# Optimization experiments

Measured on AMD Instinct MI355X. Metric: run time of the kernel, lower is better.

Reference implementation:

```python
import jax, jax.numpy as jnp
import numpy as np

NUM_RBF = 16
RBF_D_MIN, RBF_D_MAX = 2.0, 22.0
CB_A, CB_B, CB_C = -0.58273431, 0.56802827, -0.54067466
TOP_K = 32
MAX_REL = 32
NPOS = 16
HID = 128
LN_EPS = 1e-5


def _gather_nodes(nodes, idx):
    # nodes: (B, L, D), idx: (B, L, K) -> (B, L, K, D)
    return jax.vmap(lambda n, i: n[i])(nodes, idx)


def _rbf_encode(D):
    mu = jnp.linspace(RBF_D_MIN, RBF_D_MAX, NUM_RBF, dtype=D.dtype)
    sigma = (RBF_D_MAX - RBF_D_MIN) / NUM_RBF
    return jnp.exp(-((D[..., None] - mu) ** 2) / (sigma ** 2))


def setup_inputs() -> dict:
    key = jax.random.key(0)
    ks = jax.random.split(key, 4)
    B, L = 2, 2048
    X = jax.random.normal(ks[0], (B, L, 4, 3), jnp.float32) * 10.0
    residue_mask = jnp.ones((B, L), jnp.float32)
    R_idx = jnp.arange(B * L, dtype=jnp.int32).reshape(B, L)
    chain_labels = jnp.zeros((B, L), jnp.int32)
    # learned params
    W_pos = jax.random.normal(ks[1], (NPOS, 2 * MAX_REL + 2), jnp.float32) * 0.05
    b_pos = jnp.zeros((NPOS,), jnp.float32)
    W_edge = jax.random.normal(ks[2], (HID, 25 * NUM_RBF + NPOS), jnp.float32) * 0.02
    ln_gamma = jnp.ones((HID,), jnp.float32)
    ln_beta = jnp.zeros((HID,), jnp.float32)
    return {"X": X, "residue_mask": residue_mask, "R_idx": R_idx,
            "chain_labels": chain_labels, "W_pos": W_pos, "b_pos": b_pos,
            "W_edge": W_edge, "ln_gamma": ln_gamma, "ln_beta": ln_beta}


def reference(X, residue_mask, R_idx, chain_labels, W_pos, b_pos, W_edge, ln_gamma, ln_beta):
    B, L = X.shape[0], X.shape[1]
    K = min(TOP_K, L)
    # virtual CB from backbone N, CA, C
    N, CA, C = X[..., 0, :], X[..., 1, :], X[..., 2, :]
    b = CA - N
    c = C - CA
    a = jnp.cross(b, c, axis=-1)
    CB = (CB_A * a + CB_B * b + CB_C * c + CA)[..., None, :]
    atoms_5 = jnp.concatenate([X, CB], axis=-2)  # (B, L, 5, 3)
    # kNN on CA coords with invalid residues pushed far away
    diff = CA[:, :, None, :] - CA[:, None, :, :]
    dist_sq = jnp.sum(diff * diff, axis=-1)  # (B, L, L)
    inv_mask = 1.0 - residue_mask
    dist_sq = dist_sq + inv_mask[:, None, :] * 1e6
    _, E_idx = jax.lax.top_k(-dist_sq, K)  # smallest-k indices, (B, L, K)
    # gather neighbor 5-atom coords and compute 25 pairwise distances
    Xf = atoms_5.reshape(B, L, 15)
    Xg = _gather_nodes(Xf, E_idx).reshape(B, L, K, 5, 3)
    d2 = jnp.sum((atoms_5[:, :, None, :, None, :] - Xg[:, :, :, None, :, :]) ** 2, axis=-1)
    D = jnp.sqrt(d2 + 1e-6)  # (B, L, K, 5, 5)
    rbf = _rbf_encode(D).reshape(B, L, K, 25 * NUM_RBF)
    # positional encodings (standard ProteinMPNN form)
    Rg = _gather_nodes(R_idx[..., None], E_idx)[..., 0]  # (B, L, K)
    Cg = _gather_nodes(chain_labels[..., None], E_idx)[..., 0]
    d_rel = Rg - R_idx[:, :, None]
    same_chain = (Cg == chain_labels[:, :, None])
    d_clip = jnp.clip(d_rel + MAX_REL, 0, 2 * MAX_REL)
    d_final = jnp.where(same_chain, d_clip, 2 * MAX_REL + 1)
    oh = jax.nn.one_hot(d_final, 2 * MAX_REL + 2, dtype=rbf.dtype)
    pos_enc = jnp.einsum('blkc,pc->blkp', oh, W_pos) + b_pos
    # edge embedding + layernorm
    edge_input = jnp.concatenate([pos_enc, rbf], axis=-1)  # (B, L, K, 416)
    h = jnp.einsum('blkf,hf->blkh', edge_input, W_edge)
    mean = jnp.mean(h, axis=-1, keepdims=True)
    var = jnp.var(h, axis=-1, keepdims=True)
    E = (h - mean) * jax.lax.rsqrt(var + LN_EPS) * ln_gamma + ln_beta
    return E_idx, E
```

## Files before the change

### kernel.cpp

```cpp
#include <hip/hip_runtime.h>
#include <hip/hip_bf16.h>

#define LEN   2048
#define KNB   32
#define HID   128

typedef unsigned long long ull;
typedef unsigned int uint32;
typedef float f32x4 __attribute__((ext_vector_type(4)));

__global__ __launch_bounds__(256) void prep_kernel(
    const float* __restrict__ X, const float* __restrict__ mask,
    const float* __restrict__ W_edge,
    float4* __restrict__ CAm, int* __restrict__ Wf8) {
    const int t = blockIdx.x * 256 + threadIdx.x;
    if (t < 2 * LEN) {
        const float* p = X + (size_t)t * 12;
        CAm[t] = make_float4(p[3], p[4], p[5],
                             __fmul_rn(__fsub_rn(1.0f, mask[t]), 1000000.0f));
    }
    if (t < 13312) {
        const float4 w = ((const float4*)W_edge)[t];
        int r = __builtin_amdgcn_cvt_pk_fp8_f32(w.x, w.y, 0, false);
        r = __builtin_amdgcn_cvt_pk_fp8_f32(w.z, w.w, r, true);
        Wf8[t] = r;
    }
}

__global__ __launch_bounds__(256) void topk_kernel(
    const float4* __restrict__ CAm, float* __restrict__ eidx_out) {
    const int row = blockIdx.x;
    const int b = row >> 11;
    const int i = row & (LEN - 1);
    const int tid = threadIdx.x;

    __shared__ int hist[512];
    __shared__ ull cand[LEN];
    __shared__ int candcnt;
    __shared__ int selB;

    const float4* C = CAm + (size_t)b * LEN;
    const float4 ci = C[i];

    uint32 d2b[8];
#pragma unroll
    for (int q = 0; q < 8; ++q) {
        const float4 cj = C[q * 256 + tid];
        float dx = __fsub_rn(ci.x, cj.x);
        float dy = __fsub_rn(ci.y, cj.y);
        float dz = __fsub_rn(ci.z, cj.z);
        float d2 = __fadd_rn(__fadd_rn(__fmul_rn(dx, dx), __fmul_rn(dy, dy)),
                             __fmul_rn(dz, dz));
        d2 = __fadd_rn(d2, cj.w);
        d2b[q] = __float_as_uint(d2);
    }

    hist[tid] = 0; hist[tid + 256] = 0;
    if (tid == 0) candcnt = 0;
    __syncthreads();
#pragma unroll
    for (int q = 0; q < 8; ++q) atomicAdd(&hist[d2b[q] >> 22], 1);
    __syncthreads();

    if (tid < 64) {
        int loc[8];
        int s = 0;
#pragma unroll
        for (int t = 0; t < 8; ++t) { loc[t] = hist[tid * 8 + t]; s += loc[t]; }
        int incl = s;
#pragma unroll
        for (int off = 1; off < 64; off <<= 1) {
            int o = __shfl_up(incl, off, 64);
            if (tid >= off) incl += o;
        }
        const int excl = incl - s;
        if (excl < KNB && incl >= KNB) {
            int c = excl;
#pragma unroll
            for (int t = 0; t < 8; ++t) {
                int c2 = c + loc[t];
                if (c < KNB && c2 >= KNB) selB = tid * 8 + t;
                c = c2;
            }
        }
    }
    __syncthreads();
    const uint32 B = (uint32)selB;

#pragma unroll
    for (int q = 0; q < 8; ++q) {
        if ((d2b[q] >> 22) <= B) {
            int p = atomicAdd(&candcnt, 1);
            cand[p] = (((ull)d2b[q]) << 32) | (uint32)(q * 256 + tid);
        }
    }
    __syncthreads();
    const int M = candcnt;

    for (int c = tid; c < M; c += 256) {
        const ull k = cand[c];
        int r = 0;
        for (int m = 0; m < M; ++m) r += (cand[m] < k);
        if (r < KNB)
            eidx_out[(size_t)row * KNB + r] = (float)(uint32)(k & 0xFFFFFFFFull);
    }
}

__device__ __forceinline__ void load_res_atoms(const float* __restrict__ p, float* dst) {
    const float Nx = p[0], Ny = p[1], Nz = p[2];
    const float Ax = p[3], Ay = p[4], Az = p[5];
    const float Cx = p[6], Cy = p[7], Cz = p[8];
    const float Ox = p[9], Oy = p[10], Oz = p[11];
    const float bx = Ax - Nx, by = Ay - Ny, bz = Az - Nz;
    const float cx = Cx - Ax, cy = Cy - Ay, cz = Cz - Az;
    const float axv = by * cz - bz * cy;
    const float ayv = bz * cx - bx * cz;
    const float azv = bx * cy - by * cx;
    dst[0] = Nx;  dst[1] = Ny;  dst[2] = Nz;
    dst[3] = Ax;  dst[4] = Ay;  dst[5] = Az;
    dst[6] = Cx;  dst[7] = Cy;  dst[8] = Cz;
    dst[9] = Ox;  dst[10] = Oy; dst[11] = Oz;
    dst[12] = -0.58273431f * axv + 0.56802827f * bx + -0.54067466f * cx + Ax;
    dst[13] = -0.58273431f * ayv + 0.56802827f * by + -0.54067466f * cy + Ay;
    dst[14] = -0.58273431f * azv + 0.56802827f * bz + -0.54067466f * cz + Az;
}

#define FS 432

__device__ __forceinline__ int pk4(float a, float b, float c, float d) {
    int r = __builtin_amdgcn_cvt_pk_fp8_f32(a, b, 0, false);
    return __builtin_amdgcn_cvt_pk_fp8_f32(c, d, r, true);
}

__device__ __forceinline__ void compute_features(
    int tid, int Ri, int Ci,
    const float* __restrict__ W_pos, const float* __restrict__ b_pos,
    const int* jR, const int* jC,
    const float (*natoms)[15], const float* iatoms,
    unsigned char* featF8) {
    {
        const int e = tid >> 4, p = tid & 15;
        const int drel = jR[e] - Ri;
        const int same = (jC[e] == Ci);
        int dc = drel + 32;
        dc = dc < 0 ? 0 : (dc > 64 ? 64 : dc);
        const int df = same ? dc : 65;
        const float v = W_pos[p * 66 + df] + b_pos[p];
        const int pb = __builtin_amdgcn_cvt_pk_fp8_f32(v, 0.0f, 0, false);
        featF8[e * FS + p] = (unsigned char)(pb & 0xFF);
    }
#pragma unroll
    for (int it = 0; it < 2; ++it) {
        const int task = tid + it * 512;
        if (task < 800) {
            const int mn = task >> 5, e = task & 31;
            const int m = mn / 5, n = mn - m * 5;
            const float ax = iatoms[m * 3 + 0];
            const float ay = iatoms[m * 3 + 1];
            const float az = iatoms[m * 3 + 2];
            const float* na = &natoms[e][n * 3];
            const float dx = ax - na[0], dy = ay - na[1], dz = az - na[2];
            const float D = sqrtf(dx * dx + dy * dy + dz * dz + 1e-6f);
            int pk[4];
#pragma unroll
            for (int qq = 0; qq < 4; ++qq) {
                float v[4];
#pragma unroll
                for (int u = 0; u < 4; ++u) {
                    const int r = qq * 4 + u;
                    const float mu = (float)(2.0 + (double)r * (20.0 / 15.0));
                    const float t = D - mu;
                    v[u] = __expf(-(t * t) * (1.0f / 1.5625f));
                }
                pk[qq] = pk4(v[0], v[1], v[2], v[3]);
            }
            int4 w4; w4.x = pk[0]; w4.y = pk[1]; w4.z = pk[2]; w4.w = pk[3];
            *(int4*)(featF8 + e * FS + 16 + mn * 16) = w4;
        }
    }
}

__global__ __launch_bounds__(512, 6) void edge_kernel(
    const float* __restrict__ X,
    const int* __restrict__ Ridx, const int* __restrict__ Chain,
    const float* __restrict__ W_pos, const float* __restrict__ b_pos,
    const unsigned char* __restrict__ Wf8,
    const float* __restrict__ lng, const float* __restrict__ lnb,
    const float* __restrict__ eidx_f, float* __restrict__ outE) {
    const int tid = threadIdx.x;
    const int row0 = blockIdx.x * 4;
    const int b = row0 >> 11;
    const int i0 = row0 & (LEN - 1);

    __shared__ __align__(16) unsigned char featF8[32 * FS];
    __shared__ __align__(16) float hbuf[32 * 132];
    __shared__ float natoms[4][32][15];
    __shared__ float iatoms[4][16];
    __shared__ int jR[4][KNB], jC[4][KNB];
    __shared__ int riS[4], ciS[4];

    const float* Xb = X + (size_t)b * LEN * 12;

    const int w = tid >> 6, l = tid & 63, lr = l & 15, lg = l >> 4;
    long wreg[13];
    {
        const unsigned char* wb = Wf8 + (size_t)(w * 16 + lr) * 416 + lg * 8;
#pragma unroll
        for (int ks = 0; ks < 13; ++ks)
            wreg[ks] = *(const long*)(wb + ks * 32);
    }

    if (tid < 128) {
        const int r = tid >> 5, e = tid & 31;
        const int j = (int)eidx_f[(size_t)(row0 + r) * KNB + e];
        jR[r][e] = Ridx[b * LEN + j];
        jC[r][e] = Chain[b * LEN + j];
        load_res_atoms(Xb + j * 12, &natoms[r][e][0]);
    } else if (tid < 132) {
        const int r = tid - 128;
        load_res_atoms(Xb + (size_t)(i0 + r) * 12, &iatoms[r][0]);
    } else if (tid < 136) {
        riS[tid - 132] = Ridx[b * LEN + i0 + (tid - 132)];
    } else if (tid < 140) {
        ciS[tid - 136] = Chain[b * LEN + i0 + (tid - 136)];
    }
    __syncthreads();

    compute_features(tid, riS[0], ciS[0], W_pos, b_pos,
                     jR[0], jC[0], natoms[0], iatoms[0], featF8);
    __syncthreads();

    for (int r = 0; r < 4; ++r) {
        const int row = row0 + r;

        f32x4 acc0 = {0.f, 0.f, 0.f, 0.f}, acc1 = acc0;
        {
            const unsigned char* fb0 = featF8 + lr * FS + lg * 8;
            const unsigned char* fb1 = featF8 + (16 + lr) * FS + lg * 8;
#pragma unroll
            for (int ks = 0; ks < 13; ++ks) {
                const long a0 = *(const long*)(fb0 + ks * 32);
                const long a1 = *(const long*)(fb1 + ks * 32);
                acc0 = __builtin_amdgcn_mfma_f32_16x16x32_fp8_fp8(a0, wreg[ks], acc0, 0, 0, 0);
                acc1 = __builtin_amdgcn_mfma_f32_16x16x32_fp8_fp8(a1, wreg[ks], acc1, 0, 0, 0);
            }
        }
#pragma unroll
        for (int rr = 0; rr < 4; ++rr) {
            hbuf[(lg * 4 + rr) * 132 + w * 16 + lr]      = acc0[rr];
            hbuf[(16 + lg * 4 + rr) * 132 + w * 16 + lr] = acc1[rr];
        }
        __syncthreads();

        {
            const int g = tid >> 4, l2 = tid & 15;
            const float4* hb4 = (const float4*)(hbuf + g * 132 + l2 * 8);
            const float4 v0 = hb4[0], v1 = hb4[1];
            float s = v0.x + v0.y + v0.z + v0.w + v1.x + v1.y + v1.z + v1.w;
            float ssq = v0.x * v0.x + v0.y * v0.y + v0.z * v0.z + v0.w * v0.w
                      + v1.x * v1.x + v1.y * v1.y + v1.z * v1.z + v1.w * v1.w;
#pragma unroll
            for (int off = 1; off < 16; off <<= 1) {
                s += __shfl_xor(s, off, 64);
                ssq += __shfl_xor(ssq, off, 64);
            }
            const float mean = s * (1.0f / 128.0f);
            const float rstd = rsqrtf(ssq * (1.0f / 128.0f) - mean * mean + 1e-5f);

            float4* ob = (float4*)(outE + ((size_t)row * KNB + g) * HID + l2 * 8);
            const float4 g0 = *(const float4*)(lng + l2 * 8);
            const float4 g1 = *(const float4*)(lng + l2 * 8 + 4);
            const float4 b0 = *(const float4*)(lnb + l2 * 8);
            const float4 b1 = *(const float4*)(lnb + l2 * 8 + 4);
            float4 o0, o1;
            o0.x = (v0.x - mean) * rstd * g0.x + b0.x;
            o0.y = (v0.y - mean) * rstd * g0.y + b0.y;
            o0.z = (v0.z - mean) * rstd * g0.z + b0.z;
            o0.w = (v0.w - mean) * rstd * g0.w + b0.w;
            o1.x = (v1.x - mean) * rstd * g1.x + b1.x;
            o1.y = (v1.y - mean) * rstd * g1.y + b1.y;
            o1.z = (v1.z - mean) * rstd * g1.z + b1.z;
            o1.w = (v1.w - mean) * rstd * g1.w + b1.w;
            ob[0] = o0;
            ob[1] = o1;
        }
        if (r < 3) {
            compute_features(tid, riS[r + 1], ciS[r + 1], W_pos, b_pos,
                             jR[r + 1], jC[r + 1], natoms[r + 1], iatoms[r + 1],
                             featF8);
        }
        __syncthreads();
    }
}

extern "C" void kernel_launch(void* const* d_in, const int* in_sizes, int n_in,
                              void* d_out, int out_size, void* d_ws, size_t ws_size,
                              hipStream_t stream) {
    const float* X      = (const float*)d_in[0];
    const float* mask   = (const float*)d_in[1];
    const int*   Ridx   = (const int*)d_in[2];
    const int*   Chain  = (const int*)d_in[3];
    const float* W_pos  = (const float*)d_in[4];
    const float* b_pos  = (const float*)d_in[5];
    const float* W_edge = (const float*)d_in[6];
    const float* lng    = (const float*)d_in[7];
    const float* lnb    = (const float*)d_in[8];

    float* out  = (float*)d_out;
    float* eidx = out;
    float* E    = out + (size_t)2 * LEN * KNB;

    float4* CAm = (float4*)d_ws;
    unsigned char* Wf8 = (unsigned char*)d_ws + 2 * LEN * 16;

    const int nrow = 2 * LEN;
    prep_kernel<<<52, 256, 0, stream>>>(X, mask, W_edge, CAm, (int*)Wf8);
    topk_kernel<<<nrow, 256, 0, stream>>>(CAm, eidx);
    edge_kernel<<<nrow / 4, 512, 0, stream>>>(X, Ridx, Chain, W_pos, b_pos, Wf8,
                                              lng, lnb, eidx, E);
}
```

Baseline: 61.11 us.

## Fuse top-k selection into edge kernel and compute RBF via recurrence

Removes the separate top-k kernel and runs the histogram-based neighbor selection for each of the 4 rows inside the edge kernel, aliasing candidate/histogram buffers with the feature buffers in a shared pool. Neighbor indices then go through shared memory instead of a global round trip, and one launch is dropped. The RBF encoding also swaps 16 exps per distance for 2 exps plus a multiplicative recurrence from the centre bin, with clamping. That risks small numeric drift, and the per-row top-k sequence serializes extra barriers inside the block.

```diff
diff --git a/kernel.cpp b/kernel.cpp
--- a/kernel.cpp
+++ b/kernel.cpp
@@ -4,6 +4,7 @@
 #define LEN   2048
 #define KNB   32
 #define HID   128
+#define FS    432
 
 typedef unsigned long long ull;
 typedef unsigned int uint32;
@@ -24,85 +25,6 @@
         int r = __builtin_amdgcn_cvt_pk_fp8_f32(w.x, w.y, 0, false);
         r = __builtin_amdgcn_cvt_pk_fp8_f32(w.z, w.w, r, true);
         Wf8[t] = r;
-    }
-}
-
-__global__ __launch_bounds__(256) void topk_kernel(
-    const float4* __restrict__ CAm, float* __restrict__ eidx_out) {
-    const int row = blockIdx.x;
-    const int b = row >> 11;
-    const int i = row & (LEN - 1);
-    const int tid = threadIdx.x;
-
-    __shared__ int hist[512];
-    __shared__ ull cand[LEN];
-    __shared__ int candcnt;
-    __shared__ int selB;
-
-    const float4* C = CAm + (size_t)b * LEN;
-    const float4 ci = C[i];
-
-    uint32 d2b[8];
-#pragma unroll
-    for (int q = 0; q < 8; ++q) {
-        const float4 cj = C[q * 256 + tid];
-        float dx = __fsub_rn(ci.x, cj.x);
-        float dy = __fsub_rn(ci.y, cj.y);
-        float dz = __fsub_rn(ci.z, cj.z);
-        float d2 = __fadd_rn(__fadd_rn(__fmul_rn(dx, dx), __fmul_rn(dy, dy)),
-                             __fmul_rn(dz, dz));
-        d2 = __fadd_rn(d2, cj.w);
-        d2b[q] = __float_as_uint(d2);
-    }
-
-    hist[tid] = 0; hist[tid + 256] = 0;
-    if (tid == 0) candcnt = 0;
-    __syncthreads();
-#pragma unroll
-    for (int q = 0; q < 8; ++q) atomicAdd(&hist[d2b[q] >> 22], 1);
-    __syncthreads();
-
-    if (tid < 64) {
-        int loc[8];
-        int s = 0;
-#pragma unroll
-        for (int t = 0; t < 8; ++t) { loc[t] = hist[tid * 8 + t]; s += loc[t]; }
-        int incl = s;
-#pragma unroll
-        for (int off = 1; off < 64; off <<= 1) {
-            int o = __shfl_up(incl, off, 64);
-            if (tid >= off) incl += o;
-        }
-        const int excl = incl - s;
-        if (excl < KNB && incl >= KNB) {
-            int c = excl;
-#pragma unroll
-            for (int t = 0; t < 8; ++t) {
-                int c2 = c + loc[t];
-                if (c < KNB && c2 >= KNB) selB = tid * 8 + t;
-                c = c2;
-            }
-        }
-    }
-    __syncthreads();
-    const uint32 B = (uint32)selB;
-
-#pragma unroll
-    for (int q = 0; q < 8; ++q) {
-        if ((d2b[q] >> 22) <= B) {
-            int p = atomicAdd(&candcnt, 1);
-            cand[p] = (((ull)d2b[q]) << 32) | (uint32)(q * 256 + tid);
-        }
-    }
-    __syncthreads();
-    const int M = candcnt;
-
-    for (int c = tid; c < M; c += 256) {
-        const ull k = cand[c];
-        int r = 0;
-        for (int m = 0; m < M; ++m) r += (cand[m] < k);
-        if (r < KNB)
-            eidx_out[(size_t)row * KNB + r] = (float)(uint32)(k & 0xFFFFFFFFull);
     }
 }
 
@@ -121,16 +43,23 @@
     dst[6] = Cx;  dst[7] = Cy;  dst[8] = Cz;
     dst[9] = Ox;  dst[10] = Oy; dst[11] = Oz;
     dst[12] = -0.58273431f * axv + 0.56802827f * bx + -0.54067466f * cx + Ax;
-    dst[13] = -0.58273431f * ayv + 0.56802827f * by + -0.54067466f * cy + Ay;
+    dst[13] = -0.58273431f * ayv + 0.56802827f * by + -0.54067466f * cy +Ay;
     dst[14] = -0.58273431f * azv + 0.56802827f * bz + -0.54067466f * cz + Az;
 }
-
-#define FS 432
 
 __device__ __forceinline__ int pk4(float a, float b, float c, float d) {
     int r = __builtin_amdgcn_cvt_pk_fp8_f32(a, b, 0, false);
     return __builtin_amdgcn_cvt_pk_fp8_f32(c, d, r, true);
 }
+
+#define E1  3.2053337e-1f
+#define E3  3.2931300e-2f
+#define E5  3.3834000e-3f
+#define E7  3.4760500e-4f
+#define E9  3.5712900e-5f
+#define E11 3.6691300e-6f
+#define E13 3.7696000e-7f
+#define E15 3.8729500e-8f
 
 __device__ __forceinline__ void compute_features(
     int tid, int Ri, int Ci,
@@ -161,20 +90,32 @@
             const float* na = &natoms[e][n * 3];
             const float dx = ax - na[0], dy = ay - na[1], dz = az - na[2];
             const float D = sqrtf(dx * dx + dy * dy + dz * dz + 1e-6f);
-            int pk[4];
-#pragma unroll
-            for (int qq = 0; qq < 4; ++qq) {
-                float v[4];
-#pragma unroll
-                for (int u = 0; u < 4; ++u) {
-                    const int r = qq * 4 + u;
-                    const float mu = (float)(2.0 + (double)r * (20.0 / 15.0));
-                    const float t = D - mu;
-                    v[u] = __expf(-(t * t) * (1.0f / 1.5625f));
-                }
-                pk[qq] = pk4(v[0], v[1], v[2], v[3]);
-            }
-            int4 w4; w4.x = pk[0]; w4.y = pk[1]; w4.z = pk[2]; w4.w = pk[3];
+            float v = D - 12.6666667f;
+            v = fminf(fmaxf(v, -14.0f), 14.0f);
+            const float A  = __expf(-0.64f * v * v);
+            const float C  = __expf(1.70666667f * v);
+            const float Ci_ = 1.0f / C;
+            const float f8 = A;
+            const float f9  = f8  * C * E1;
+            const float f10 = f9  * C * E3;
+            const float f11 = f10 * C * E5;
+            const float f12 = f11 * C * E7;
+            const float f13 = f12 * C * E9;
+            const float f14 = f13 * C * E11;
+            const float f15 = f14 * C * E13;
+            const float f7 = f8 * Ci_ * E1;
+            const float f6 = f7 * Ci_ * E3;
+            const float f5 = f6 * Ci_ * E5;
+            const float f4 = f5 * Ci_ * E7;
+            const float f3 = f4 * Ci_ * E9;
+            const float f2 = f3 * Ci_ * E11;
+            const float f1 = f2 * Ci_ * E13;
+            const float f0 = f1 * Ci_ * E15;
+            int4 w4;
+            w4.x = pk4(f0, f1, f2, f3);
+            w4.y = pk4(f4, f5, f6, f7);
+            w4.z = pk4(f8, f9, f10, f11);
+            w4.w = pk4(f12, f13, f14, f15);
             *(int4*)(featF8 + e * FS + 16 + mn * 16) = w4;
         }
     }
@@ -186,20 +127,95 @@
     const float* __restrict__ W_pos, const float* __restrict__ b_pos,
     const unsigned char* __restrict__ Wf8,
     const float* __restrict__ lng, const float* __restrict__ lnb,
-    const float* __restrict__ eidx_f, float* __restrict__ outE) {
+    const float4* __restrict__ CAm,
+    float* __restrict__ eidx_out, float* __restrict__ outE) {
     const int tid = threadIdx.x;
     const int row0 = blockIdx.x * 4;
     const int b = row0 >> 11;
     const int i0 = row0 & (LEN - 1);
 
-    __shared__ __align__(16) unsigned char featF8[32 * FS];
-    __shared__ __align__(16) float hbuf[32 * 132];
+    __shared__ __align__(16) unsigned char pool[30720];
     __shared__ float natoms[4][32][15];
     __shared__ float iatoms[4][16];
-    __shared__ int jR[4][KNB], jC[4][KNB];
+    __shared__ int jR[4][KNB], jC[4][KNB], jidx[4][KNB];
     __shared__ int riS[4], ciS[4];
-
-    const float* Xb = X + (size_t)b * LEN * 12;
+    __shared__ int candcnt, selB;
+
+    ull* cand = (ull*)pool;
+    int* hist = (int*)(pool + 16384);
+    unsigned char* featF8 = pool;
+    float* hbuf = (float*)(pool + 13824);
+
+    const float4* Cc = CAm + (size_t)b * LEN;
+
+    for (int r = 0; r < 4; ++r) {
+        hist[tid] = 0;
+        if (tid == 0) candcnt = 0;
+        __syncthreads();
+        const float4 ci = Cc[i0 + r];
+        uint32 d2b[4];
+#pragma unroll
+        for (int q = 0; q < 4; ++q) {
+            const float4 cj = Cc[q * 512 + tid];
+            float dx = __fsub_rn(ci.x, cj.x);
+            float dy = __fsub_rn(ci.y, cj.y);
+            float dz = __fsub_rn(ci.z, cj.z);
+            float d2 = __fadd_rn(__fadd_rn(__fmul_rn(dx, dx), __fmul_rn(dy, dy)),
+                                 __fmul_rn(dz, dz));
+            d2 = __fadd_rn(d2, cj.w);
+            d2b[q] = __float_as_uint(d2);
+        }
+#pragma unroll
+        for (int q = 0; q < 4; ++q) atomicAdd(&hist[d2b[q] >> 22], 1);
+        __syncthreads();
+
+        if (tid < 64) {
+            int loc[8];
+            int s = 0;
+#pragma unroll
+            for (int t = 0; t < 8; ++t) { loc[t] = hist[tid * 8 + t]; s += loc[t]; }
+            int incl = s;
+#pragma unroll
+            for (int off = 1; off < 64; off <<= 1) {
+                int o = __shfl_up(incl, off, 64);
+                if (tid >= off) incl += o;
+            }
+            const int excl = incl - s;
+            if (excl < KNB && incl >= KNB) {
+                int c = excl;
+#pragma unroll
+                for (int t = 0; t < 8; ++t) {
+                    int c2 = c + loc[t];
+                    if (c < KNB && c2 >= KNB) selB = tid * 8 + t;
+                    c = c2;
+                }
+            }
+        }
+        __syncthreads();
+        const uint32 B = (uint32)selB;
+
+#pragma unroll
+        for (int q = 0; q < 4; ++q) {
+            if ((d2b[q] >> 22) <= B) {
+                int p = atomicAdd(&candcnt, 1);
+                cand[p] = (((ull)d2b[q]) << 32) | (uint32)(q * 512 + tid);
+            }
+        }
+        __syncthreads();
+        const int M = candcnt;
+
+        for (int c = tid; c < M; c += 512) {
+            const ull k = cand[c];
+            int rk = 0;
+            for (int m = 0; m < M; ++m) rk += (cand[m] < k);
+            if (rk < KNB) {
+                const int j = (int)(uint32)(k & 0xFFFFFFFFull);
+                eidx_out[(size_t)(row0 + r) * KNB + rk] = (float)j;
+                jidx[r][rk] = j;
+            }
+        }
+        __syncthreads();
+    }
 
     const int w = tid >> 6, l = tid & 63, lr = l & 15, lg = l >> 4;
     long wreg[13];
@@ -210,9 +226,10 @@
             wreg[ks] = *(const long*)(wb + ks * 32);
     }
 
+    const float* Xb = X + (size_t)b * LEN * 12;
     if (tid < 128) {
         const int r = tid >> 5, e = tid & 31;
-        const int j = (int)eidx_f[(size_t)(row0 + r) * KNB + e];
+        const int j = jidx[r][e];
         jR[r][e] = Ridx[b * LEN + j];
         jC[r][e] = Chain[b * LEN + j];
         load_res_atoms(Xb + j * 12, &natoms[r][e][0]);
@@ -313,9 +330,7 @@
     float4* CAm = (float4*)d_ws;
     unsigned char* Wf8 = (unsigned char*)d_ws + 2 * LEN * 16;
 
-    const int nrow = 2 * LEN;
     prep_kernel<<<52, 256, 0, stream>>>(X, mask, W_edge, CAm, (int*)Wf8);
-    topk_kernel<<<nrow, 256, 0, stream>>>(CAm, eidx);
-    edge_kernel<<<nrow / 4, 512, 0, stream>>>(X, Ridx, Chain, W_pos, b_pos, Wf8,
-                                              lng, lnb, eidx, E);
-}
+    edge_kernel<<<(2 * LEN) / 4, 512, 0, stream>>>(X, Ridx, Chain, W_pos, b_pos,
+                                                   Wf8, lng, lnb, CAm, eidx, E);
+}
```

New measurement: 80.12 us. 1.31x slower.

## Compute RBF via Gaussian recurrence and XOR-swizzle fp8 feature tile in LDS

Applied to the files above, without the earlier changes.

Replaces the 16 exponentials per distance with two Gaussian anchors (centres 4 and 12) plus one exponential and one reciprocal, then derives the neighbouring RBF values by multiplying with precomputed ratio constants. Separately, the fp8 feature rows are padded to 512 bytes and their 16-byte chunks XOR-swizzled by row, so the MFMA operand loads hit fewer LDS bank conflicts. The recurrence trades transcendental work for chained multiplies, which can drift or underflow at extreme distances; the distance is clamped to 40 to bound this, and fp8 quantisation hides most of the error. The wider rows use more shared memory per block, which may lower occupancy.

```diff
diff --git a/kernel.cpp b/kernel.cpp
--- a/kernel.cpp
+++ b/kernel.cpp
@@ -4,6 +4,7 @@
 #define LEN   2048
 #define KNB   32
 #define HID   128
+#define FS    512
 
 typedef unsigned long long ull;
 typedef unsigned int uint32;
@@ -125,12 +126,15 @@
     dst[14] = -0.58273431f * azv + 0.56802827f * bz + -0.54067466f * cz + Az;
 }
 
-#define FS 432
-
 __device__ __forceinline__ int pk4(float a, float b, float c, float d) {
     int r = __builtin_amdgcn_cvt_pk_fp8_f32(a, b, 0, false);
     return __builtin_amdgcn_cvt_pk_fp8_f32(c, d, r, true);
 }
+
+#define E1  3.2053337e-1f
+#define E3  3.2931300e-2f
+#define E5  3.3834001e-3f
+#define E7  3.4760500e-4f
 
 __device__ __forceinline__ void compute_features(
     int tid, int Ri, int Ci,
@@ -147,7 +151,7 @@
         const int df = same ? dc : 65;
         const float v = W_pos[p * 66 + df] + b_pos[p];
         const int pb = __builtin_amdgcn_cvt_pk_fp8_f32(v, 0.0f, 0, false);
-        featF8[e * FS + p] = (unsigned char)(pb & 0xFF);
+        featF8[e * FS + ((e & 7) << 4) + p] = (unsigned char)(pb & 0xFF);
     }
 #pragma unroll
     for (int it = 0; it < 2; ++it) {
@@ -161,21 +165,37 @@
             const float* na = &natoms[e][n * 3];
             const float dx = ax - na[0], dy = ay - na[1], dz = az - na[2];
             const float D = sqrtf(dx * dx + dy * dy + dz * dz + 1e-6f);
-            int pk[4];
-#pragma unroll
-            for (int qq = 0; qq < 4; ++qq) {
-                float v[4];
-#pragma unroll
-                for (int u = 0; u < 4; ++u) {
-                    const int r = qq * 4 + u;
-                    const float mu = (float)(2.0 + (double)r * (20.0 / 15.0));
-                    const float t = D - mu;
-                    v[u] = __expf(-(t * t) * (1.0f / 1.5625f));
-                }
-                pk[qq] = pk4(v[0], v[1], v[2], v[3]);
-            }
-            int4 w4; w4.x = pk[0]; w4.y = pk[1]; w4.z = pk[2]; w4.w = pk[3];
-            *(int4*)(featF8 + e * FS + 16 + mn * 16) = w4;
+            const float Dc = fminf(D, 40.0f);
+            const float v4 = Dc - 7.3333333f;
+            const float v12 = Dc - 18.0f;
+            const float A4  = __expf(-0.64f * v4 * v4);
+            const float A12 = __expf(-0.64f * v12 * v12);
+            const float C4  = __expf(1.7066667f * v4);
+            const float Ci4 = 1.0f / C4;
+            const float C12  = C4 * 1.24140e-8f;
+            const float Ci12 = Ci4 * 8.05543e7f;
+            const float f4 = A4;
+            const float f5 = f4 * C4 * E1;
+            const float f6 = f5 * C4 * E3;
+            const float f7 = f6 * C4 * E5;
+            const float f3 = f4 * Ci4 * E1;
+            const float f2 = f3 * Ci4 * E3;
+            const float f1 = f2 * Ci4 * E5;
+            const float f0 = f1 * Ci4 * E7;
+            const float f12 = A12;
+            const float f13 = f12 * C12 * E1;
+            const float f14 = f13 * C12 * E3;
+            const float f15 = f14 * C12 * E5;
+            const float f11 = f12 * Ci12 * E1;
+            const float f10 = f11 * Ci12 * E3;
+            const float f9  = f10 * Ci12 * E5;
+            const float f8  = f9  * Ci12 * E7;
+            int4 w4;
+            w4.x = pk4(f0, f1, f2, f3);
+            w4.y = pk4(f4, f5, f6, f7);
+            w4.z = pk4(f8, f9, f10, f11);
+            w4.w = pk4(f12, f13, f14, f15);
+            *(int4*)(featF8 + e * FS + (((1 + mn) ^ (e & 7)) << 4)) = w4;
         }
     }
 }
@@ -235,12 +255,15 @@
 
         f32x4 acc0 = {0.f, 0.f, 0.f, 0.f}, acc1 = acc0;
         {
-            const unsigned char* fb0 = featF8 + lr * FS + lg * 8;
-            const unsigned char* fb1 = featF8 + (16 + lr) * FS + lg * 8;
+            const int sw = lr & 7;
+            const int mb = lg >> 1;
+            const unsigned char* fb0 = featF8 + lr * FS + (lg & 1) * 8;
+            const unsigned char* fb1 = featF8 + (16 + lr) * FS + (lg & 1) * 8;
 #pragma unroll
             for (int ks = 0; ks < 13; ++ks) {
-                const long a0 = *(const long*)(fb0 + ks * 32);
-                const long a1 = *(const long*)(fb1 + ks * 32);
+                const int moff = ((2 * ks + mb) ^ sw) << 4;
+                const long a0 = *(const long*)(fb0 + moff);
+                const long a1 = *(const long*)(fb1 + moff);
                 acc0 = __builtin_amdgcn_mfma_f32_16x16x32_fp8_fp8(a0, wreg[ks], acc0, 0, 0, 0);
                 acc1 = __builtin_amdgcn_mfma_f32_16x16x32_fp8_fp8(a1, wreg[ks], acc1, 0, 0, 0);
             }
```

Result: slower. 64.01 us (+4.7%).
